# Kernel tuning notes

Hardware: AMD Instinct MI355X
Metric: run time of the kernel (lower is better)

The kernel has to match this reference:

```python
import jax, jax.numpy as jnp
import numpy as np

B, T, IN, H = 1024, 128, 5, 100  # batch, seq_len, input_size, hidden_size


def setup_inputs() -> dict:
    key = jax.random.key(0)
    ks = jax.random.split(key, 20)
    bound = 1.0 / np.sqrt(H)  # PyTorch LSTM init: U(-1/sqrt(H), 1/sqrt(H))

    def u(k, shape):
        return jax.random.uniform(k, shape, jnp.float32, -bound, bound)

    inp = {"x": jax.random.normal(ks[0], (B, T, IN), jnp.float32)}
    i = 1
    for layer, din in [(0, IN), (1, 2 * H)]:
        for d in ("f", "b"):
            inp[f"w_ih_l{layer}{d}"] = u(ks[i], (4 * H, din)); i += 1
            inp[f"w_hh_l{layer}{d}"] = u(ks[i], (4 * H, H)); i += 1
            inp[f"b_ih_l{layer}{d}"] = u(ks[i], (4 * H,)); i += 1
            inp[f"b_hh_l{layer}{d}"] = u(ks[i], (4 * H,)); i += 1
    inp["fc_w"] = u(ks[17], (3, 2 * H))
    inp["fc_b"] = u(ks[18], (3,))
    return inp


def _run_dir(x, w_ih, w_hh, b_ih, b_hh, reverse):
    """One LSTM direction. x: [B,T,D] -> hidden seq [B,T,H]. PyTorch gate order i,f,g,o."""
    xT = jnp.swapaxes(x, 0, 1)  # [T,B,D]
    # precompute input contribution for all timesteps: [T,B,4H]
    xg = jnp.einsum('tbd,gd->tbg', xT, w_ih) + b_ih + b_hh

    def step(carry, g_in):
        h, c = carry
        g = g_in + h @ w_hh.T  # [B,4H]
        i, f, gg, o = jnp.split(g, 4, axis=-1)
        c = jax.nn.sigmoid(f) * c + jax.nn.sigmoid(i) * jnp.tanh(gg)
        h = jax.nn.sigmoid(o) * jnp.tanh(c)
        return (h, c), h

    b = x.shape[0]
    init = (jnp.zeros((b, H), x.dtype), jnp.zeros((b, H), x.dtype))
    _, hs = jax.lax.scan(step, init, xg, reverse=reverse)  # hs[t] aligned with time t
    return jnp.swapaxes(hs, 0, 1)  # [B,T,H]


def reference(x,
              w_ih_l0f, w_hh_l0f, b_ih_l0f, b_hh_l0f,
              w_ih_l0b, w_hh_l0b, b_ih_l0b, b_hh_l0b,
              w_ih_l1f, w_hh_l1f, b_ih_l1f, b_hh_l1f,
              w_ih_l1b, w_hh_l1b, b_ih_l1b, b_hh_l1b,
              fc_w, fc_b):
    # Layer 0 (bidirectional): [B,T,2H]
    h0 = jnp.concatenate([
        _run_dir(x, w_ih_l0f, w_hh_l0f, b_ih_l0f, b_hh_l0f, False),
        _run_dir(x, w_ih_l0b, w_hh_l0b, b_ih_l0b, b_hh_l0b, True),
    ], axis=-1)
    # (inter-layer dropout p=0.2 is identity in eval mode)
    # Layer 1 (bidirectional): [B,T,2H]
    h1 = jnp.concatenate([
        _run_dir(h0, w_ih_l1f, w_hh_l1f, b_ih_l1f, b_hh_l1f, False),
        _run_dir(h0, w_ih_l1b, w_hh_l1b, b_ih_l1b, b_hh_l1b, True),
    ], axis=-1)
    last = h1[:, -1, :]  # [B,2H]
    # (dropout p=0.5 is identity in eval mode)
    logits = last @ fc_w.T + fc_b  # [B,3]
    return jax.nn.softmax(logits, axis=1)
```

## Files before the change

kernel.cpp:

```cpp
#include <hip/hip_runtime.h>
#include <hip/hip_fp16.h>


typedef __attribute__((ext_vector_type(8))) short bf16x8;
typedef __attribute__((ext_vector_type(4))) float f32x4;

constexpr int Bsz = 1024, Tt = 128, IN_ = 5, H = 100, G = 400, D1 = 200;
constexpr int NP = 512;
constexpr int NT = 25;
constexpr int MB = 8;
constexpr int MB1 = 4;
constexpr int NGRP = 4;
constexpr int GSTRIDE = 512;

__device__ __forceinline__ float sigm(float x)   { return 1.f / (1.f + __expf(-x)); }
__device__ __forceinline__ float tanhf_(float x) { return 1.f - 2.f / (__expf(2.f * x) + 1.f); }
__device__ __forceinline__ unsigned short f2bf(float f) {
  unsigned u = __float_as_uint(f);
  u += 0x7fff + ((u >> 16) & 1);
  return (unsigned short)(u >> 16);
}

__device__ __forceinline__ void pack_body(
    const float* wA, int KA, const float* wB, int KB, int kbo,
    const float* b1, const float* b2, int bias_k,
    unsigned short* dst, int Kg, int idx) {
  if (idx >= Kg * NP * 8) return;
  int jj = idx & 7, rest = idx >> 3;
  int np_ = rest % NP, g = rest / NP;
  int j = np_ >> 2, gate = np_ & 3;
  int k = g * 8 + jj;
  float v = 0.f;
  if (j < H) {
    int n = gate * H + j;
    if (k < KA) v = wA[n * KA + k];
    else if (KB > 0 && k >= kbo && k < kbo + KB) v = wB[n * KB + (k - kbo)];
    else if (k == bias_k) v = b1[n] + b2[n];
  }
  dst[idx] = f2bf(v);
}

__global__ void pack_all(
    const float* __restrict__ w_hh_l0f, const float* __restrict__ w_ih_l0f,
    const float* __restrict__ b_ih_l0f, const float* __restrict__ b_hh_l0f,
    const float* __restrict__ w_hh_l0b, const float* __restrict__ w_ih_l0b,
    const float* __restrict__ b_ih_l0b, const float* __restrict__ b_hh_l0b,
    const float* __restrict__ w_hh_l1f, const float* __restrict__ b_ih_l1f,
    const float* __restrict__ b_hh_l1f,
    const float* __restrict__ w_ih_l1f, const float* __restrict__ w_ih_l1b,
    const float* __restrict__ b_ih_l1b, const float* __restrict__ b_hh_l1b,
    unsigned short* __restrict__ pk0f, unsigned short* __restrict__ pk0b,
    unsigned short* __restrict__ pkhh, unsigned short* __restrict__ pkxg,
    unsigned short* __restrict__ pk1b) {
  int idx = blockIdx.x * 256 + threadIdx.x;
  switch (blockIdx.y) {
    case 0: pack_body(w_hh_l0f, 100, w_ih_l0f, 5, 100, b_ih_l0f, b_hh_l0f, 105, pk0f, 16, idx); break;
    case 1: pack_body(w_hh_l0b, 100, w_ih_l0b, 5, 100, b_ih_l0b, b_hh_l0b, 105, pk0b, 16, idx); break;
    case 2: pack_body(w_hh_l1f, 100, nullptr, 0, 0, b_ih_l1f, b_hh_l1f, -1, pkhh, 16, idx); break;
    case 3: pack_body(w_ih_l1f, 200, nullptr, 0, 0, b_ih_l1f, b_hh_l1f, 200, pkxg, 28, idx); break;
    default: pack_body(w_ih_l1b, 200, nullptr, 0, 0, b_ih_l1b, b_hh_l1b, 200, pk1b, 28, idx);
  }
}

__global__ __launch_bounds__(1024, 1) void lstm_l0(
    const float* __restrict__ x,
    const unsigned short* __restrict__ pk_f, const unsigned short* __restrict__ pk_b,
    unsigned short* __restrict__ h0fT, unsigned short* __restrict__ h0bT) {
  __shared__ __align__(16) short A_s[2][16][16][8];

  const int tid = threadIdx.x;
  const int lane = tid & 63, w = tid >> 6;
  const int q = lane >> 4, l16 = lane & 15;
  const int b0 = blockIdx.x * MB;
  const int dir = blockIdx.y;
  const unsigned short* pk = dir ? pk_b : pk_f;
  unsigned short* hT = dir ? h0bT : h0fT;

  for (int i = tid; i < 2 * 16 * 16 * 8; i += 1024) ((short*)A_s)[i] = 0;

  const int mtA = w, mtB = w + 16;
  const bool bvalid = (mtB < NT);
  bf16x8 wfA[4], wfB[4];
#pragma unroll
  for (int kt = 0; kt < 4; ++kt) {
    wfA[kt] = *(const bf16x8*)(pk + ((size_t)(kt * 4 + q) * NP + mtA * 16 + l16) * 8);
    wfB[kt] = *(const bf16x8*)(pk + ((size_t)(kt * 4 + q) * NP + mtB * 16 + l16) * 8);
  }
  float c = 0.f;
  const bool up = (l16 >= 8);
  const int mm = l16 & 7;
  const int j = (up ? mtB : mtA) * 4 + q;
  const bool valid = up ? bvalid : true;
  const int xm = tid / IN_, xe = tid - xm * IN_;
  const int sm = tid / 25, sj = (tid - (tid / 25) * 25) * 4;
  const float* xp = x + ((size_t)(b0 + xm) * Tt + (dir ? Tt - 2 : 1)) * IN_ + xe;
  const int xstride = dir ? -IN_ : IN_;
  unsigned short* hp =
      hT + ((size_t)(dir ? Tt - 1 : 0) * Bsz + b0 + sm) * H + sj;
  const int hstride = dir ? -(Bsz * H) : (Bsz * H);
  __syncthreads();
  if (tid < 16) {
    A_s[0][13][tid][1] = (short)f2bf(1.f);
    A_s[1][13][tid][1] = (short)f2bf(1.f);
  }
  if (tid < MB * IN_) {
    int t0 = dir ? (Tt - 1) : 0;
    int k = 100 + xe;
    short xv = (short)f2bf(x[((size_t)(b0 + xm) * Tt + t0) * IN_ + xe]);
    A_s[0][k >> 3][xm][k & 7] = xv;
    A_s[0][k >> 3][xm + 8][k & 7] = xv;
  }
  __syncthreads();

  int p = 0;
  for (int step = 0; step < Tt; ++step) {
    if (step > 0 && tid < 200) {
      uint2 hv = *(const uint2*)&A_s[p][sj >> 3][sm][sj & 7];
      *(uint2*)hp = hv;
      hp += hstride;
    }
    float xn = 0.f;
    const bool do_x = (tid < MB * IN_) && (step < Tt - 1);
    if (do_x) { xn = *xp; xp += xstride; }
    bf16x8 hfrag[4];
#pragma unroll
    for (int kt = 0; kt < 4; ++kt) hfrag[kt] = *(const bf16x8*)A_s[p][kt * 4 + q][l16];
    f32x4 accA = (f32x4){0.f, 0.f, 0.f, 0.f};
    f32x4 accB = (f32x4){0.f, 0.f, 0.f, 0.f};
#pragma unroll
    for (int kt = 0; kt < 4; ++kt)
      accA = __builtin_amdgcn_mfma_f32_16x16x32_bf16(wfA[kt], hfrag[kt], accA, 0, 0, 0);
    if (bvalid) {
#pragma unroll
      for (int kt = 0; kt < 4; ++kt)
        accB = __builtin_amdgcn_mfma_f32_16x16x32_bf16(wfB[kt], hfrag[kt], accB, 0, 0, 0);
    }
    float g0 = up ? accB[0] : accA[0];
    float g1 = up ? accB[1] : accA[1];
    float g2 = up ? accB[2] : accA[2];
    float g3 = up ? accB[3] : accA[3];
    float cc = sigm(g1) * c + sigm(g0) * tanhf_(g2);
    c = cc;
    float h = sigm(g3) * tanhf_(cc);
    if (valid) {
      short hh = (short)f2bf(h);
      A_s[1 - p][j >> 3][mm][j & 7] = hh;
      A_s[1 - p][j >> 3][mm + 8][j & 7] = hh;
    }
    if (do_x) {
      int k = 100 + xe;
      short xv = (short)f2bf(xn);
      A_s[1 - p][k >> 3][xm][k & 7] = xv;
      A_s[1 - p][k >> 3][xm + 8][k & 7] = xv;
    }
    __syncthreads();
    p ^= 1;
  }
  if (tid < 200) *(uint2*)hp = *(const uint2*)&A_s[p][sj >> 3][sm][sj & 7];
}

__global__ __launch_bounds__(1024, 1) void gemm_xg(
    const unsigned short* __restrict__ h0fT, const unsigned short* __restrict__ h0bT,
    const unsigned short* __restrict__ pkw, __half* __restrict__ xg) {
  __shared__ __align__(16) short B_s[2][28][64][8];
  const int tid = threadIdx.x;
  const int lane = tid & 63, w = tid >> 6;
  const int q = lane >> 4, l16 = lane & 15;

#pragma unroll
  for (int b = 0; b < 2; ++b)
    for (int i = tid; i < 3 * 64 * 8; i += 1024) {
      int jj = i & 7, gl = i >> 9;
      ((short*)&B_s[b][25][0][0])[i] = (short)((gl == 0 && jj == 0) ? f2bf(1.f) : 0);
    }

  const int mtA = w, mtB = w + 16;
  const bool bvalid = (mtB < NT);
  bf16x8 wfA[7], wfB[7];
#pragma unroll
  for (int kt = 0; kt < 7; ++kt) {
    wfA[kt] = *(const bf16x8*)(pkw + ((size_t)(kt * 4 + q) * NP + mtA * 16 + l16) * 8);
    wfB[kt] = *(const bf16x8*)(pkw + ((size_t)(kt * 4 + q) * NP + mtB * 16 + l16) * 8);
  }
  const int jA = mtA * 4 + q, jB = mtB * 4 + q;

  const int t0m = tid / 25, t0j = (tid - t0m * 25) * 4;
  const int t1 = tid + 1024;
  const int t1m = t1 / 25, t1j = (t1 - t1m * 25) * 4;
  uint2 sf0, sb0, sf1, sb1;

#define XG_ISSUE(GRP)                                                  \
  {                                                                    \
    size_t base_ = (size_t)(GRP)*64 * H;                               \
    sf0 = *(const uint2*)(h0fT + base_ + t0m * H + t0j);               \
    sb0 = *(const uint2*)(h0bT + base_ + t0m * H + t0j);               \
    if (tid < 576) {                                                   \
      sf1 = *(const uint2*)(h0fT + base_ + t1m * H + t1j);             \
      sb1 = *(const uint2*)(h0bT + base_ + t1m * H + t1j);             \
    }                                                                  \
  }
#define XG_COMMIT(BUF)                                                 \
  {                                                                    \
    *(uint2*)&B_s[BUF][t0j >> 3][t0m][t0j & 7] = sf0;                  \
    int k0_ = 100 + t0j;                                               \
    *(uint2*)&B_s[BUF][k0_ >> 3][t0m][k0_ & 7] = sb0;                  \
    if (tid < 576) {                                                   \
      *(uint2*)&B_s[BUF][t1j >> 3][t1m][t1j & 7] = sf1;                \
      int k1_ = 100 + t1j;                                             \
      *(uint2*)&B_s[BUF][k1_ >> 3][t1m][k1_ & 7] = sb1;                \
    }                                                                  \
  }

  const int g0 = blockIdx.x;
  XG_ISSUE(g0);
  XG_COMMIT(0);
  __syncthreads();

  for (int i = 0; i < NGRP; ++i) {
    if (i < NGRP - 1) XG_ISSUE(g0 + GSTRIDE * (i + 1));
    const short(*Bb)[64][8] = B_s[i & 1];
    const int r0 = (g0 + GSTRIDE * i) * 64;
#pragma unroll
    for (int rg = 0; rg < 4; ++rg) {
      f32x4 accA = (f32x4){0.f, 0.f, 0.f, 0.f};
      f32x4 accB = (f32x4){0.f, 0.f, 0.f, 0.f};
#pragma unroll
      for (int kt = 0; kt < 7; ++kt) {
        bf16x8 hf = *(const bf16x8*)Bb[kt * 4 + q][rg * 16 + l16];
        accA = __builtin_amdgcn_mfma_f32_16x16x32_bf16(wfA[kt], hf, accA, 0, 0, 0);
        if (bvalid)
          accB = __builtin_amdgcn_mfma_f32_16x16x32_bf16(wfB[kt], hf, accB, 0, 0, 0);
      }
      const size_t row = (size_t)(r0 + rg * 16 + l16);
      {
        __half2 h01 = __floats2half2_rn(accA[0], accA[1]);
        __half2 h23 = __floats2half2_rn(accA[2], accA[3]);
        uint2 st; *(__half2*)&st.x = h01; *(__half2*)&st.y = h23;
        *(uint2*)(xg + row * G + 4 * jA) = st;
      }
      if (bvalid) {
        __half2 h01 = __floats2half2_rn(accB[0], accB[1]);
        __half2 h23 = __floats2half2_rn(accB[2], accB[3]);
        uint2 st; *(__half2*)&st.x = h01; *(__half2*)&st.y = h23;
        *(uint2*)(xg + row * G + 4 * jB) = st;
      }
    }
    if (i < NGRP - 1) XG_COMMIT((i & 1) ^ 1);
    __syncthreads();
  }
#undef XG_ISSUE
#undef XG_COMMIT
}

__global__ __launch_bounds__(1024, 1) void lstm_l1(
    const unsigned short* __restrict__ h0fT, const unsigned short* __restrict__ h0bT,
    const unsigned short* __restrict__ pk_hh, const unsigned short* __restrict__ pk1b,
    const __half* __restrict__ xg,
    const float* __restrict__ fc_w, const float* __restrict__ fc_b,
    float* __restrict__ out) {
  __shared__ __align__(16) short A_s[2][16][16][8];
  __shared__ __align__(16) short A2_s[28][16][8];
  __shared__ float hf_s[MB1][H];
  __shared__ float hb_s[MB1][H];
  __shared__ float fcw_s[3 * D1];
  __shared__ float fcb_s[3];
  __shared__ float logit_s[MB1][3];

  const int tid = threadIdx.x;
  const int lane = tid & 63, w = tid >> 6;
  const int q = lane >> 4, l16 = lane & 15;
  const int b0 = blockIdx.x * MB1;
  const uint2* xg2 = (const uint2*)xg;

  for (int i = tid; i < 2 * 16 * 16 * 8; i += 1024) ((short*)A_s)[i] = 0;
  for (int i = tid; i < 25 * 16 * 8; i += 1024) ((short*)A2_s)[i] = 0;
  for (int i = tid; i < 3 * 16 * 8; i += 1024) {
    int jj = i & 7, gl = i >> 7;
    ((short*)&A2_s[25][0][0])[i] = (short)((gl == 0 && jj == 0) ? f2bf(1.f) : 0);
  }
  for (int i = tid; i < 3 * D1; i += 1024) fcw_s[i] = fc_w[i];
  if (tid < 3) fcb_s[tid] = fc_b[tid];

  const bool busy = (w < 7);
  const int m = l16 & 3, g16 = l16 >> 2;
  const int myMt = w * 4 + g16;
  const int jme = myMt * 4 + q;
  const bool evalid = busy && (myMt < NT);
  int mts[4]; bool tv[4];
  bf16x8 wf[4][4];
  if (busy) {
#pragma unroll
    for (int i = 0; i < 4; ++i) {
      int mt = w * 4 + i; mts[i] = mt; tv[i] = (mt < NT);
#pragma unroll
      for (int kt = 0; kt < 4; ++kt)
        wf[i][kt] = *(const bf16x8*)(pk_hh + ((size_t)(kt * 4 + q) * NP + mt * 16 + l16) * 8);
    }
  }
  float c = 0.f;
  const uint2* xgp = xg2 + (size_t)(b0 + m) * 100 + jme;
  uint2 xgCur = {0, 0};
  if (busy) { xgCur = *xgp; xgp += Bsz * 100; }
  __syncthreads();

  int p = 0;
  for (int t = 0; t < Tt; ++t) {
    if (busy) {
      uint2 xgNxt = xgCur;
      if (t < Tt - 1) { xgNxt = *xgp; xgp += Bsz * 100; }
      bf16x8 hfrag[4];
#pragma unroll
      for (int kt = 0; kt < 4; ++kt) hfrag[kt] = *(const bf16x8*)A_s[p][kt * 4 + q][l16];
      f32x4 acc[4];
#pragma unroll
      for (int i = 0; i < 4; ++i) {
        acc[i] = (f32x4){0.f, 0.f, 0.f, 0.f};
        if (!tv[i]) continue;
#pragma unroll
        for (int kt = 0; kt < 4; ++kt)
          acc[i] = __builtin_amdgcn_mfma_f32_16x16x32_bf16(wf[i][kt], hfrag[kt], acc[i], 0, 0, 0);
      }
      float2 x01 = __half22float2(*(const __half2*)&xgCur.x);
      float2 x23 = __half22float2(*(const __half2*)&xgCur.y);
      float xr[4] = {x01.x, x01.y, x23.x, x23.y};
      float gr[4];
#pragma unroll
      for (int r = 0; r < 4; ++r) {
        float lo = (g16 & 1) ? acc[1][r] : acc[0][r];
        float hi = (g16 & 1) ? acc[3][r] : acc[2][r];
        gr[r] = ((g16 & 2) ? hi : lo) + xr[r];
      }
      float cc = sigm(gr[1]) * c + sigm(gr[0]) * tanhf_(gr[2]);
      c = cc;
      float h = sigm(gr[3]) * tanhf_(cc);
      if (evalid) {
        short hh = (short)f2bf(h);
        A_s[1 - p][jme >> 3][m][jme & 7] = hh;
        A_s[1 - p][jme >> 3][m + 4][jme & 7] = hh;
        A_s[1 - p][jme >> 3][m + 8][jme & 7] = hh;
        A_s[1 - p][jme >> 3][m + 12][jme & 7] = hh;
        if (t == Tt - 1) hf_s[m][jme] = h;
      }
      xgCur = xgNxt;
    }
    __syncthreads();
    p ^= 1;
  }

  {
    const size_t base = ((size_t)(Tt - 1) * Bsz + b0) * H;
    if (tid < 100) {
      int m2 = tid / 25, j0 = (tid - (tid / 25) * 25) * 4;
      *(uint2*)&A2_s[j0 >> 3][m2][j0 & 7] = *(const uint2*)(h0fT + base + m2 * H + j0);
      int k = 100 + j0;
      *(uint2*)&A2_s[k >> 3][m2][k & 7] = *(const uint2*)(h0bT + base + m2 * H + j0);
    }
  }
  __syncthreads();
  if (busy) {
    f32x4 acc[4];
#pragma unroll
    for (int i = 0; i < 4; ++i) acc[i] = (f32x4){0.f, 0.f, 0.f, 0.f};
#pragma unroll
    for (int kt = 0; kt < 7; ++kt) {
      bf16x8 hf = *(const bf16x8*)A2_s[kt * 4 + q][l16 & 3];
#pragma unroll
      for (int i = 0; i < 4; ++i) {
        if (!tv[i]) continue;
        bf16x8 wfb = *(const bf16x8*)(pk1b + ((size_t)(kt * 4 + q) * NP + mts[i] * 16 + l16) * 8);
        acc[i] = __builtin_amdgcn_mfma_f32_16x16x32_bf16(wfb, hf, acc[i], 0, 0, 0);
      }
    }
    float gr[4];
#pragma unroll
    for (int r = 0; r < 4; ++r) {
      float lo = (g16 & 1) ? acc[1][r] : acc[0][r];
      float hi = (g16 & 1) ? acc[3][r] : acc[2][r];
      gr[r] = (g16 & 2) ? hi : lo;
    }
    float cc = sigm(gr[0]) * tanhf_(gr[2]);
    if (evalid) hb_s[m][jme] = sigm(gr[3]) * tanhf_(cc);
  }
  __syncthreads();

  if (tid < MB1 * 3) {
    int mr = tid / 3, cls = tid - mr * 3;
    float s = fcb_s[cls];
    for (int jj = 0; jj < H; ++jj) s += fcw_s[cls * D1 + jj] * hf_s[mr][jj];
    for (int jj = 0; jj < H; ++jj) s += fcw_s[cls * D1 + H + jj] * hb_s[mr][jj];
    logit_s[mr][cls] = s;
  }
  __syncthreads();
  if (tid < MB1) {
    float a = logit_s[tid][0], b = logit_s[tid][1], cc = logit_s[tid][2];
    float mx = fmaxf(a, fmaxf(b, cc));
    float e0 = __expf(a - mx), e1 = __expf(b - mx), e2 = __expf(cc - mx);
    float inv = 1.f / (e0 + e1 + e2);
    out[(b0 + tid) * 3 + 0] = e0 * inv;
    out[(b0 + tid) * 3 + 1] = e1 * inv;
    out[(b0 + tid) * 3 + 2] = e2 * inv;
  }
}

extern "C" void kernel_launch(void* const* d_in, const int* in_sizes, int n_in,
                              void* d_out, int out_size, void* d_ws, size_t ws_size,
                              hipStream_t stream) {
  const float* x        = (const float*)d_in[0];
  const float* w_ih_l0f = (const float*)d_in[1];
  const float* w_hh_l0f = (const float*)d_in[2];
  const float* b_ih_l0f = (const float*)d_in[3];
  const float* b_hh_l0f = (const float*)d_in[4];
  const float* w_ih_l0b = (const float*)d_in[5];
  const float* w_hh_l0b = (const float*)d_in[6];
  const float* b_ih_l0b = (const float*)d_in[7];
  const float* b_hh_l0b = (const float*)d_in[8];
  const float* w_ih_l1f = (const float*)d_in[9];
  const float* w_hh_l1f = (const float*)d_in[10];
  const float* b_ih_l1f = (const float*)d_in[11];
  const float* b_hh_l1f = (const float*)d_in[12];
  const float* w_ih_l1b = (const float*)d_in[13];
  const float* b_ih_l1b = (const float*)d_in[15];
  const float* b_hh_l1b = (const float*)d_in[16];
  const float* fc_w     = (const float*)d_in[17];
  const float* fc_b     = (const float*)d_in[18];

  unsigned short* h0fT = (unsigned short*)d_ws;
  unsigned short* h0bT = h0fT + (size_t)Tt * Bsz * H;
  __half* xgT          = (__half*)(h0bT + (size_t)Tt * Bsz * H);
  unsigned short* pk0f = (unsigned short*)(xgT + (size_t)Tt * Bsz * G);
  unsigned short* pk0b = pk0f + 16 * NP * 8;
  unsigned short* pkhh = pk0b + 16 * NP * 8;
  unsigned short* pkxg = pkhh + 16 * NP * 8;
  unsigned short* pk1b = pkxg + 28 * NP * 8;

  pack_all<<<dim3(448, 5), 256, 0, stream>>>(
      w_hh_l0f, w_ih_l0f, b_ih_l0f, b_hh_l0f,
      w_hh_l0b, w_ih_l0b, b_ih_l0b, b_hh_l0b,
      w_hh_l1f, b_ih_l1f, b_hh_l1f,
      w_ih_l1f, w_ih_l1b, b_ih_l1b, b_hh_l1b,
      pk0f, pk0b, pkhh, pkxg, pk1b);

  lstm_l0<<<dim3(Bsz / MB, 2), 1024, 0, stream>>>(x, pk0f, pk0b, h0fT, h0bT);
  gemm_xg<<<GSTRIDE, 1024, 0, stream>>>(h0fT, h0bT, pkxg, xgT);
  lstm_l1<<<Bsz / MB1, 1024, 0, stream>>>(h0fT, h0bT, pkhh, pk1b, xgT,
                                          fc_w, fc_b, (float*)d_out);
}
```

Baseline: 358.4 us.

## Concentrate layer-0 recurrent MFMA work into 7 waves with 4 tiles each

The layer-0 recurrent kernel now assigns four 16-row weight tiles to each of the first 7 waves, instead of spreading two tiles across all 16 waves. The h-state store and x-load duties move to otherwise idle waves. Each active wave now shares one LDS fragment load across four MFMAs and updates two cells per lane. The aim is to cut redundant LDS reads and give the memory side-work its own waves. The cost is a longer serial MFMA chain per wave each timestep, which could lengthen the critical path of the recurrence.

```diff
diff --git a/kernel.cpp b/kernel.cpp
--- a/kernel.cpp
+++ b/kernel.cpp
@@ -78,21 +78,32 @@
 
   for (int i = tid; i < 2 * 16 * 16 * 8; i += 1024) ((short*)A_s)[i] = 0;
 
-  const int mtA = w, mtB = w + 16;
-  const bool bvalid = (mtB < NT);
-  bf16x8 wfA[4], wfB[4];
-#pragma unroll
-  for (int kt = 0; kt < 4; ++kt) {
-    wfA[kt] = *(const bf16x8*)(pk + ((size_t)(kt * 4 + q) * NP + mtA * 16 + l16) * 8);
-    wfB[kt] = *(const bf16x8*)(pk + ((size_t)(kt * 4 + q) * NP + mtB * 16 + l16) * 8);
-  }
-  float c = 0.f;
-  const bool up = (l16 >= 8);
-  const int mm = l16 & 7;
-  const int j = (up ? mtB : mtA) * 4 + q;
-  const bool valid = up ? bvalid : true;
-  const int xm = tid / IN_, xe = tid - xm * IN_;
-  const int sm = tid / 25, sj = (tid - (tid / 25) * 25) * 4;
+  const bool busy = (w < 7);
+  const bool hi = (l16 >= 8);
+  const int row = l16 & 7;
+  bf16x8 wf[4][4];
+  if (busy) {
+#pragma unroll
+    for (int i = 0; i < 4; ++i) {
+      int mt = w * 4 + i;
+#pragma unroll
+      for (int kt = 0; kt < 4; ++kt)
+        wf[i][kt] = *(const bf16x8*)(pk + ((size_t)(kt * 4 + q) * NP + mt * 16 + l16) * 8);
+    }
+  }
+  const int mt0 = w * 4 + (hi ? 2 : 0);
+  const int j0 = mt0 * 4 + q, j1 = j0 + 4;
+  const bool v0 = busy && (mt0 < NT);
+  const bool v1 = busy && (mt0 + 1 < NT);
+  float c0 = 0.f, c1 = 0.f;
+
+  const int st = tid - 448;
+  const bool sl = (st >= 0 && st < 200);
+  const int sm = sl ? st / 25 : 0, sj = sl ? (st - (st / 25) * 25) * 4 : 0;
+  const int xt = tid - 704;
+  const bool xl = (xt >= 0 && xt < MB * IN_);
+  const int xm = xl ? xt / IN_ : 0;
+  const int xe = xl ? xt - xm * IN_ : 0;
   const float* xp = x + ((size_t)(b0 + xm) * Tt + (dir ? Tt - 2 : 1)) * IN_ + xe;
   const int xstride = dir ? -IN_ : IN_;
   unsigned short* hp =
@@ -103,7 +114,7 @@
     A_s[0][13][tid][1] = (short)f2bf(1.f);
     A_s[1][13][tid][1] = (short)f2bf(1.f);
   }
-  if (tid < MB * IN_) {
+  if (xl) {
     int t0 = dir ? (Tt - 1) : 0;
     int k = 100 + xe;
     short xv = (short)f2bf(x[((size_t)(b0 + xm) * Tt + t0) * IN_ + xe]);
@@ -114,38 +125,47 @@
 
   int p = 0;
   for (int step = 0; step < Tt; ++step) {
-    if (step > 0 && tid < 200) {
+    if (step > 0 && sl) {
       uint2 hv = *(const uint2*)&A_s[p][sj >> 3][sm][sj & 7];
       *(uint2*)hp = hv;
       hp += hstride;
     }
     float xn = 0.f;
-    const bool do_x = (tid < MB * IN_) && (step < Tt - 1);
+    const bool do_x = xl && (step < Tt - 1);
     if (do_x) { xn = *xp; xp += xstride; }
-    bf16x8 hfrag[4];
-#pragma unroll
-    for (int kt = 0; kt < 4; ++kt) hfrag[kt] = *(const bf16x8*)A_s[p][kt * 4 + q][l16];
-    f32x4 accA = (f32x4){0.f, 0.f, 0.f, 0.f};
-    f32x4 accB = (f32x4){0.f, 0.f, 0.f, 0.f};
-#pragma unroll
-    for (int kt = 0; kt < 4; ++kt)
-      accA = __builtin_amdgcn_mfma_f32_16x16x32_bf16(wfA[kt], hfrag[kt], accA, 0, 0, 0);
-    if (bvalid) {
-#pragma unroll
-      for (int kt = 0; kt < 4; ++kt)
-        accB = __builtin_amdgcn_mfma_f32_16x16x32_bf16(wfB[kt], hfrag[kt], accB, 0, 0, 0);
-    }
-    float g0 = up ? accB[0] : accA[0];
-    float g1 = up ? accB[1] : accA[1];
-    float g2 = up ? accB[2] : accA[2];
-    float g3 = up ? accB[3] : accA[3];
-    float cc = sigm(g1) * c + sigm(g0) * tanhf_(g2);
-    c = cc;
-    float h = sigm(g3) * tanhf_(cc);
-    if (valid) {
-      short hh = (short)f2bf(h);
-      A_s[1 - p][j >> 3][mm][j & 7] = hh;
-      A_s[1 - p][j >> 3][mm + 8][j & 7] = hh;
+    if (busy) {
+      f32x4 acc0 = (f32x4){0.f, 0.f, 0.f, 0.f};
+      f32x4 acc1 = (f32x4){0.f, 0.f, 0.f, 0.f};
+      f32x4 acc2 = (f32x4){0.f, 0.f, 0.f, 0.f};
+      f32x4 acc3 = (f32x4){0.f, 0.f, 0.f, 0.f};
+#pragma unroll
+      for (int kt = 0; kt < 4; ++kt) {
+        bf16x8 hf = *(const bf16x8*)A_s[p][kt * 4 + q][l16];
+        acc0 = __builtin_amdgcn_mfma_f32_16x16x32_bf16(wf[0][kt], hf, acc0, 0, 0, 0);
+        acc1 = __builtin_amdgcn_mfma_f32_16x16x32_bf16(wf[1][kt], hf, acc1, 0, 0, 0);
+        acc2 = __builtin_amdgcn_mfma_f32_16x16x32_bf16(wf[2][kt], hf, acc2, 0, 0, 0);
+        acc3 = __builtin_amdgcn_mfma_f32_16x16x32_bf16(wf[3][kt], hf, acc3, 0, 0, 0);
+      }
+      float gA0 = hi ? acc2[0] : acc0[0], gA1 = hi ? acc2[1] : acc0[1];
+      float gA2 = hi ? acc2[2] : acc0[2], gA3 = hi ? acc2[3] : acc0[3];
+      float gB0 = hi ? acc3[0] : acc1[0], gB1 = hi ? acc3[1] : acc1[1];
+      float gB2 = hi ? acc3[2] : acc1[2], gB3 = hi ? acc3[3] : acc1[3];
+      float cc0 = sigm(gA1) * c0 + sigm(gA0) * tanhf_(gA2);
+      c0 = cc0;
+      float h0v = sigm(gA3) * tanhf_(cc0);
+      float cc1 = sigm(gB1) * c1 + sigm(gB0) * tanhf_(gB2);
+      c1 = cc1;
+      float h1v = sigm(gB3) * tanhf_(cc1);
+      if (v0) {
+        short hh = (short)f2bf(h0v);
+        A_s[1 - p][j0 >> 3][row][j0 & 7] = hh;
+        A_s[1 - p][j0 >> 3][row + 8][j0 & 7] = hh;
+      }
+      if (v1) {
+        short hh = (short)f2bf(h1v);
+        A_s[1 - p][j1 >> 3][row][j1 & 7] = hh;
+        A_s[1 - p][j1 >> 3][row + 8][j1 & 7] = hh;
+      }
     }
     if (do_x) {
       int k = 100 + xe;
@@ -156,7 +176,7 @@
     __syncthreads();
     p ^= 1;
   }
-  if (tid < 200) *(uint2*)hp = *(const uint2*)&A_s[p][sj >> 3][sm][sj & 7];
+  if (sl) *(uint2*)hp = *(const uint2*)&A_s[p][sj >> 3][sm][sj & 7];
 }
 
 __global__ __launch_bounds__(1024, 1) void gemm_xg(
```

Result: no change. 357.5 us (-0.2%).
